# Performance work log

Measured on AMD Instinct MI355X. Metric: run time of the kernel, lower is better.

Reference implementation:

```python
import jax, jax.numpy as jnp
import numpy as np

BETA_MEM = 0.9
BETA_INH = 0.6
THRESHOLD = 1.0  # snn.Leaky default


def setup_inputs() -> dict:
    key = jax.random.key(0)
    k1, = jax.random.split(key, 1)
    T, B = 1024, 16384
    spike_seq = (jax.random.uniform(k1, (T, B, 2)) < 0.05).astype(jnp.float32)
    w_exc = jnp.array([[0.7, 1.0]], dtype=jnp.float32)  # fc_exc.weight, [1, 2]
    w_inh = jnp.array(-1.0, dtype=jnp.float32)          # scalar inhibitory weight
    return {"spike_seq": spike_seq, "w_exc": w_exc, "w_inh": w_inh}


@jax.custom_vjp
def spike_fn(x):
    # Heaviside spike with ATan surrogate gradient (snntorch default, alpha=2)
    return (x > 0).astype(x.dtype)

def _spike_fwd(x):
    return spike_fn(x), x

def _spike_bwd(x, g):
    return (g / (1.0 + (jnp.pi * x) ** 2),)

spike_fn.defvjp(_spike_fwd, _spike_bwd)


def reference(spike_seq, w_exc, w_inh):
    T, B, _ = spike_seq.shape
    mem0 = jnp.zeros((B, 1), dtype=spike_seq.dtype)
    inh0 = jnp.zeros((B, 1), dtype=spike_seq.dtype)

    def step(carry, x_t):
        mem, inh = carry
        cur_exc = x_t @ w_exc.T                      # [B, 1]
        fm1 = x_t[:, 0:1]                            # [B, 1]
        inh = BETA_INH * inh + fm1
        cur = cur_exc + w_inh * inh
        # snn.Leaky: reset (subtract) computed from previous mem, detached
        reset = jax.lax.stop_gradient((mem - THRESHOLD > 0).astype(mem.dtype))
        mem = BETA_MEM * mem + cur - reset * THRESHOLD
        spk = spike_fn(mem - THRESHOLD)
        return (mem, inh), (spk, mem)

    _, (spk_rec, mem_rec) = jax.lax.scan(step, (mem0, inh0), spike_seq)
    return spk_rec, mem_rec  # each [T, B, 1]
```

## Files before the change

### kernel.cpp

```cpp
#include <hip/hip_runtime.h>

#define T_LEN  1024
#define B_N    16384
#define CHUNKS 32
#define CLEN   (T_LEN / CHUNKS)
#define TPW    16
#define NTC    (T_LEN / TPW)
#define PF     8

__device__ __forceinline__ void neuron_step(float x0, float x1,
                                            float w0, float w1, float wi,
                                            float& mem, float& inh, float& spk) {
#pragma clang fp contract(off)
  const float cur_exc = x0 * w0 + x1 * w1;
  inh = 0.6f * inh + x0;
  const float cur = cur_exc + wi * inh;
  const float reset = (mem - 1.0f > 0.0f) ? 1.0f : 0.0f;
  mem = 0.9f * mem + cur - reset * 1.0f;
  spk = (mem - 1.0f > 0.0f) ? 1.0f : 0.0f;
}

__global__ __launch_bounds__(256) void FMFM_pack(
    const float* __restrict__ x, unsigned* __restrict__ cbits) {
  const int tid = blockIdx.x * 256 + threadIdx.x;
  const int b2  = tid & (B_N / 2 - 1);
  const int tc  = tid >> 13;
  const float4* __restrict__ xp = (const float4*)x;

  unsigned bits0 = 0, bits1 = 0;
#pragma unroll
  for (int u = 0; u < TPW; ++u) {
    const int t = tc * TPW + u;
    const float4 v = xp[(size_t)t * (B_N / 2) + b2];
    bits0 |= ((v.x != 0.0f) ? 1u : 0u) << (2 * u);
    bits0 |= ((v.y != 0.0f) ? 2u : 0u) << (2 * u);
    bits1 |= ((v.z != 0.0f) ? 1u : 0u) << (2 * u);
    bits1 |= ((v.w != 0.0f) ? 2u : 0u) << (2 * u);
  }
  uint2 w; w.x = bits0; w.y = bits1;
  *(uint2*)&cbits[(size_t)tc * B_N + 2 * b2] = w;
}

__global__ __launch_bounds__(64, 1) void FMFM_scan(
    const unsigned* __restrict__ cbits, const float* __restrict__ w_exc,
    const float* __restrict__ w_inh, float* __restrict__ carry) {
#pragma clang fp contract(off)
  const int b = blockIdx.x * 64 + threadIdx.x;
  const float w0 = w_exc[0], w1 = w_exc[1], wi = w_inh[0];
  float mem = 0.0f, inh = 0.0f, spk;

  unsigned buf[PF];
#pragma unroll
  for (int i = 0; i < PF; ++i) buf[i] = cbits[i * B_N + b];

  for (int tc0 = 0; tc0 < NTC; tc0 += PF) {
#pragma unroll
    for (int i = 0; i < PF; ++i) {
      const int tc = tc0 + i;
      if ((tc & 1) == 0) {
        const int c = tc >> 1;
        carry[c * B_N + b] = mem;
        carry[(CHUNKS + c) * B_N + b] = inh;
      }
      const unsigned w = buf[i];
      int nx = tc + PF; if (nx > NTC - 1) nx = NTC - 1;
      buf[i] = cbits[nx * B_N + b];
#pragma unroll
      for (int u = 0; u < TPW; ++u) {
        const float x0 = (float)((w >> (2 * u)) & 1u);
        const float x1 = (float)((w >> (2 * u + 1)) & 1u);
        neuron_step(x0, x1, w0, w1, wi, mem, inh, spk);
      }
    }
  }
}

__global__ __launch_bounds__(256) void FMFM_emit(
    const unsigned* __restrict__ cbits, const float* __restrict__ w_exc,
    const float* __restrict__ w_inh, const float* __restrict__ carry,
    float* __restrict__ out) {
#pragma clang fp contract(off)
  const int c = blockIdx.x >> 6;
  const int b = ((blockIdx.x & 63) << 8) + threadIdx.x;
  const float w0 = w_exc[0], w1 = w_exc[1], wi = w_inh[0];

  float mem = carry[c * B_N + b];
  float inh = carry[(CHUNKS + c) * B_N + b];
  const unsigned wa = cbits[(2 * c) * B_N + b];
  const unsigned wb = cbits[(2 * c + 1) * B_N + b];

  float* __restrict__ spk_out = out;
  float* __restrict__ mem_out = out + (size_t)T_LEN * B_N;
  const int tbase = c * CLEN;
  float spk;

#pragma unroll
  for (int u = 0; u < CLEN; ++u) {
    const unsigned w = (u < TPW) ? wa : wb;
    const int s = u & (TPW - 1);
    const float x0 = (float)((w >> (2 * s)) & 1u);
    const float x1 = (float)((w >> (2 * s + 1)) & 1u);
    neuron_step(x0, x1, w0, w1, wi, mem, inh, spk);
    const int t = tbase + u;
    __builtin_nontemporal_store(spk, &spk_out[t * B_N + b]);
    __builtin_nontemporal_store(mem, &mem_out[t * B_N + b]);
  }
}

extern "C" void kernel_launch(void* const* d_in, const int* in_sizes, int n_in,
                              void* d_out, int out_size, void* d_ws, size_t ws_size,
                              hipStream_t stream) {
  const float* x     = (const float*)d_in[0];
  const float* w_exc = (const float*)d_in[1];
  const float* w_inh = (const float*)d_in[2];
  float* out = (float*)d_out;

  unsigned* cbits = (unsigned*)d_ws;
  float*    carry = (float*)((char*)d_ws + (size_t)NTC * B_N * 4);

  hipLaunchKernelGGL(FMFM_pack, dim3(NTC * (B_N / 2) / 256), dim3(256), 0,
                     stream, x, cbits);
  hipLaunchKernelGGL(FMFM_scan, dim3(B_N / 64), dim3(64), 0, stream,
                     cbits, w_exc, w_inh, carry);
  hipLaunchKernelGGL(FMFM_emit, dim3(CHUNKS * (B_N / 256)), dim3(256), 0,
                     stream, cbits, w_exc, w_inh, carry, out);
}
```

Measured before the change: 271.4 us.

## Interleave packed spike words for uint4 loads and stage scan carries in LDS

Changes the packed-bit layout so each neuron's four consecutive 16-step words sit contiguously, which lets the serial scan fetch them with one uint4 load per 64 steps using a shallow prefetch. Carry snapshots go to shared memory during the scan and are written out to global memory at the end. The per-step update drops the unused spike computation, fuses one multiply-add, and uses a select for the reset. The emit kernel reads a uint2 and switches from nontemporal to plain stores. The fused multiply-add changes rounding relative to the reference, and the pack kernel now does scattered 4-byte stores.

```diff
diff --git a/kernel.cpp b/kernel.cpp
--- a/kernel.cpp
+++ b/kernel.cpp
@@ -6,18 +6,19 @@
 #define CLEN   (T_LEN / CHUNKS)
 #define TPW    16
 #define NTC    (T_LEN / TPW)
-#define PF     8
+#define GR     (NTC / 4)
 
-__device__ __forceinline__ void neuron_step(float x0, float x1,
-                                            float w0, float w1, float wi,
-                                            float& mem, float& inh, float& spk) {
+
+__device__ __forceinline__ void neuron_step_core(float x0, float x1,
+                                                 float w0, float w1, float wi,
+                                                 float& mem, float& inh) {
 #pragma clang fp contract(off)
-  const float cur_exc = x0 * w0 + x1 * w1;
+  const float cur_exc = __builtin_fmaf(x0, w0, x1 * w1);
   inh = 0.6f * inh + x0;
   const float cur = cur_exc + wi * inh;
-  const float reset = (mem - 1.0f > 0.0f) ? 1.0f : 0.0f;
-  mem = 0.9f * mem + cur - reset * 1.0f;
-  spk = (mem - 1.0f > 0.0f) ? 1.0f : 0.0f;
+  const bool reset = (mem - 1.0f > 0.0f);
+  const float m2 = 0.9f * mem + cur;
+  mem = reset ? (m2 - 1.0f) : m2;
 }
 
 __global__ __launch_bounds__(256) void FMFM_pack(
@@ -37,8 +38,9 @@
     bits1 |= ((v.z != 0.0f) ? 1u : 0u) << (2 * u);
     bits1 |= ((v.w != 0.0f) ? 2u : 0u) << (2 * u);
   }
-  uint2 w; w.x = bits0; w.y = bits1;
-  *(uint2*)&cbits[(size_t)tc * B_N + 2 * b2] = w;
+  const size_t base = ((size_t)(tc >> 2) * B_N + 2 * b2) * 4 + (tc & 3);
+  cbits[base]     = bits0;
+  cbits[base + 4] = bits1;
 }
 
 __global__ __launch_bounds__(64, 1) void FMFM_scan(
@@ -46,32 +48,44 @@
     const float* __restrict__ w_inh, float* __restrict__ carry) {
 #pragma clang fp contract(off)
   const int b = blockIdx.x * 64 + threadIdx.x;
+  const int lt = threadIdx.x;
   const float w0 = w_exc[0], w1 = w_exc[1], wi = w_inh[0];
-  float mem = 0.0f, inh = 0.0f, spk;
+  const uint4* __restrict__ cb4 = (const uint4*)cbits;
 
-  unsigned buf[PF];
+  __shared__ float lcar[2 * CHUNKS * 64];
+
+  float mem = 0.0f, inh = 0.0f;
+
+  uint4 cur = cb4[b];
+  uint4 nxt = cb4[B_N + b];
+
+  for (int g = 0; g < GR; ++g) {
+    const int gp = (g + 2 < GR) ? (g + 2) : (GR - 1);
+    const uint4 pf = cb4[(size_t)gp * B_N + b];
+    unsigned ws[4] = {cur.x, cur.y, cur.z, cur.w};
 #pragma unroll
-  for (int i = 0; i < PF; ++i) buf[i] = cbits[i * B_N + b];
-
-  for (int tc0 = 0; tc0 < NTC; tc0 += PF) {
-#pragma unroll
-    for (int i = 0; i < PF; ++i) {
-      const int tc = tc0 + i;
-      if ((tc & 1) == 0) {
-        const int c = tc >> 1;
-        carry[c * B_N + b] = mem;
-        carry[(CHUNKS + c) * B_N + b] = inh;
+    for (int j = 0; j < 4; ++j) {
+      if ((j & 1) == 0) {
+        const int c = 2 * g + (j >> 1);
+        lcar[(2 * c + 0) * 64 + lt] = mem;
+        lcar[(2 * c + 1) * 64 + lt] = inh;
       }
-      const unsigned w = buf[i];
-      int nx = tc + PF; if (nx > NTC - 1) nx = NTC - 1;
-      buf[i] = cbits[nx * B_N + b];
+      const unsigned w = ws[j];
 #pragma unroll
       for (int u = 0; u < TPW; ++u) {
         const float x0 = (float)((w >> (2 * u)) & 1u);
         const float x1 = (float)((w >> (2 * u + 1)) & 1u);
-        neuron_step(x0, x1, w0, w1, wi, mem, inh, spk);
+        neuron_step_core(x0, x1, w0, w1, wi, mem, inh);
       }
     }
+    cur = nxt;
+    nxt = pf;
+  }
+
+#pragma unroll
+  for (int c = 0; c < CHUNKS; ++c) {
+    carry[c * B_N + b]            = lcar[(2 * c + 0) * 64 + lt];
+    carry[(CHUNKS + c) * B_N + b] = lcar[(2 * c + 1) * 64 + lt];
   }
 }
 
@@ -86,13 +100,13 @@
 
   float mem = carry[c * B_N + b];
   float inh = carry[(CHUNKS + c) * B_N + b];
-  const unsigned wa = cbits[(2 * c) * B_N + b];
-  const unsigned wb = cbits[(2 * c + 1) * B_N + b];
+  const uint2 wv = *(const uint2*)&cbits[((size_t)(c >> 1) * B_N + b) * 4 +
+                                         (c & 1) * 2];
+  const unsigned wa = wv.x, wb = wv.y;
 
   float* __restrict__ spk_out = out;
   float* __restrict__ mem_out = out + (size_t)T_LEN * B_N;
   const int tbase = c * CLEN;
-  float spk;
 
 #pragma unroll
   for (int u = 0; u < CLEN; ++u) {
@@ -100,10 +114,11 @@
     const int s = u & (TPW - 1);
     const float x0 = (float)((w >> (2 * s)) & 1u);
     const float x1 = (float)((w >> (2 * s + 1)) & 1u);
-    neuron_step(x0, x1, w0, w1, wi, mem, inh, spk);
+    neuron_step_core(x0, x1, w0, w1, wi, mem, inh);
+    const float spk = (mem - 1.0f > 0.0f) ? 1.0f : 0.0f;
     const int t = tbase + u;
-    __builtin_nontemporal_store(spk, &spk_out[t * B_N + b]);
-    __builtin_nontemporal_store(mem, &mem_out[t * B_N + b]);
+    spk_out[t * B_N + b] = spk;
+    mem_out[t * B_N + b] = mem;
   }
 }
 
```

New measurement: 269.1 us. Within noise of the previous version (-0.8%).
